# Optimization experiments

Hardware: AMD Instinct MI355X
Metric: run time of the kernel (lower is better)

The kernel has to match this reference:

```python
import jax, jax.numpy as jnp
import numpy as np

B, N, E = 2, 10000, 160000
D, DC, L = 512, 8, 3
EPS = 1e-5


def layer_norm(x, g, b):
    m = jnp.mean(x, axis=-1, keepdims=True)
    v = jnp.mean((x - m) ** 2, axis=-1, keepdims=True)
    return (x - m) * jax.lax.rsqrt(v + EPS) * g + b


def setup_inputs() -> dict:
    key = jax.random.key(0)
    ks = jax.random.split(key, 8)
    node_features = jax.random.normal(ks[0], (B, N, D), dtype=jnp.float32)
    edge_index = jax.random.randint(ks[1], (2, E), 0, N, dtype=jnp.int64)
    edge_attr = jax.random.normal(ks[2], (E, D), dtype=jnp.float32)
    # manifold coordinate projection
    W_coord = jax.random.normal(ks[3], (D, DC), dtype=jnp.float32) / np.sqrt(D)
    # per-layer causal field layers (modeled as linear) and layer norms
    W_field = jax.random.normal(ks[4], (L, D, D), dtype=jnp.float32) / np.sqrt(D)
    b_field = jnp.zeros((L, D), dtype=jnp.float32)
    ln_g = jnp.ones((L, D), dtype=jnp.float32)
    ln_b = jnp.zeros((L, D), dtype=jnp.float32)
    # output projection: LayerNorm + Linear
    out_ln_g = jnp.ones((D,), dtype=jnp.float32)
    out_ln_b = jnp.zeros((D,), dtype=jnp.float32)
    W_out = jax.random.normal(ks[5], (D, D), dtype=jnp.float32) / np.sqrt(D)
    b_out = jnp.zeros((D,), dtype=jnp.float32)
    return dict(node_features=node_features, edge_index=edge_index, edge_attr=edge_attr,
                W_coord=W_coord, W_field=W_field, b_field=b_field, ln_g=ln_g, ln_b=ln_b,
                out_ln_g=out_ln_g, out_ln_b=out_ln_b, W_out=W_out, b_out=b_out)


def reference(node_features, edge_index, edge_attr, W_coord, W_field, b_field,
              ln_g, ln_b, out_ln_g, out_ln_b, W_out, b_out):
    src, dst = edge_index[0], edge_index[1]
    # node coordinates from manifold projection (computed once, from inputs)
    coords = node_features @ W_coord                        # (B, N, DC)
    # transport factor per edge, per batch: exp(-||dst_coord - src_coord||)
    coord_diff = coords[:, dst] - coords[:, src]            # (B, E, DC)
    transport = jnp.exp(-jnp.linalg.norm(coord_diff, axis=-1, keepdims=True))  # (B, E, 1)
    # degree of destination nodes (same for every batch element)
    deg = jnp.zeros((N,), dtype=node_features.dtype).at[dst].add(1.0)
    deg = jnp.clip(deg, 1.0, None)[None, :, None]           # (1, N, 1)

    x = node_features
    edge_msg = None
    for l in range(L):
        x_field = x @ W_field[l] + b_field[l]               # (B, N, D)
        # gather src features, apply transport, add edge attributes
        edge_msg = x_field[:, src] * transport + edge_attr[None]  # (B, E, D)
        # scatter-add into destination nodes, normalize by degree
        upd = jnp.zeros_like(x).at[:, dst].add(edge_msg)    # (B, N, D)
        x = layer_norm(x + upd / deg, ln_g[l], ln_b[l])
    node_output = layer_norm(x, out_ln_g, out_ln_b) @ W_out + b_out
    return node_output, edge_msg
```

## Files before the change

### kernel.cpp

```cpp
#include <hip/hip_runtime.h>
#include <stdint.h>

#define NN 10000
#define EE 160000
#define BB 2
#define DD 512
#define KC 1024
#define MVALID 20000
#define MPAD 20096
#define LEPS 1e-5f

typedef __bf16 bf16_t;
typedef __bf16 bf16x8 __attribute__((ext_vector_type(8)));
typedef __bf16 bf16x4 __attribute__((ext_vector_type(4)));
typedef float f32x4 __attribute__((ext_vector_type(4)));
typedef float f32x2 __attribute__((ext_vector_type(2)));

__device__ inline void gload16(const void* g, void* l) {
  __builtin_amdgcn_global_load_lds((const __attribute__((address_space(1))) uint32_t*)g,
                                   (__attribute__((address_space(3))) uint32_t*)l,
                                   16, 0, 0);
}

__global__ __launch_bounds__(256) void convw_k(const float* __restrict__ Wf,
                                               const float* __restrict__ Wo,
                                               bf16_t* __restrict__ wcat) {
  __shared__ float tile[64][65];
  const int kt = blockIdx.x, nt = blockIdx.y, l = blockIdx.z;
  const float* W = (l < 3) ? (Wf + (size_t)l * 262144) : Wo;
  const int tn = threadIdx.x & 63;
  const int tk = threadIdx.x >> 6;
#pragma unroll
  for (int i = 0; i < 16; i++) {
    const int kl = tk + i * 4;
    tile[kl][tn] = W[(size_t)(kt * 64 + kl) * 512 + nt * 64 + tn];
  }
  __syncthreads();
  const int kl2 = threadIdx.x & 63;
  const int nb = threadIdx.x >> 6;
#pragma unroll
  for (int i = 0; i < 16; i++) {
    const int nl = nb + i * 4;
    bf16_t h = (bf16_t)tile[kl2][nl];
    size_t o = ((size_t)l * 512 + nt * 64 + nl) * 1024 + kt * 64 + kl2;
    wcat[o] = h;
    wcat[o + 512] = h;
  }
}

__global__ __launch_bounds__(256) void coords_k(const float* __restrict__ x,
                                                const float* __restrict__ Wc,
                                                float* __restrict__ out,
                                                bf16_t* __restrict__ xcat) {
  __shared__ float smW[DD * 8];
  for (int i = threadIdx.x; i < DD * 8; i += 256) smW[i] = Wc[i];
  __syncthreads();
  const int wave = threadIdx.x >> 6, lane = threadIdx.x & 63;
  const int n = blockIdx.x * 4 + wave;
  const int b = blockIdx.y;
  const size_t row = (size_t)b * NN + n;
  const float* xr = x + row * DD + lane * 8;
  f32x4 x0 = *(const f32x4*)xr;
  f32x4 x1 = *(const f32x4*)(xr + 4);
  bf16x8 hi, lo;
#pragma unroll
  for (int j = 0; j < 8; j++) {
    float v = (j < 4) ? x0[j] : x1[j - 4];
    bf16_t h = (bf16_t)v;
    hi[j] = h;
    lo[j] = (bf16_t)(v - (float)h);
  }
  bf16_t* xc = xcat + row * KC + lane * 8;
  *(bf16x8*)xc = hi;
  *(bf16x8*)(xc + DD) = lo;
  float a[8];
#pragma unroll
  for (int dc = 0; dc < 8; dc++) a[dc] = 0.f;
#pragma unroll
  for (int j = 0; j < 8; j++) {
    float xv = (j < 4) ? x0[j] : x1[j - 4];
    const float* wrow = smW + (lane * 8 + j) * 8;
#pragma unroll
    for (int dc = 0; dc < 8; dc++) a[dc] += xv * wrow[dc];
  }
#pragma unroll
  for (int dc = 0; dc < 8; dc++)
    for (int o = 32; o >= 1; o >>= 1) a[dc] += __shfl_xor(a[dc], o);
  if (lane == 0) {
#pragma unroll
    for (int dc = 0; dc < 8; dc++) out[row * 8 + dc] = a[dc];
  }
}

__global__ __launch_bounds__(256) void transport_deg_k(const float* __restrict__ coords,
                                                       const int* __restrict__ srcA,
                                                       const int* __restrict__ dstA,
                                                       float* __restrict__ tr,
                                                       int* __restrict__ degc) {
  int e = blockIdx.x * 256 + threadIdx.x;
  int s = srcA[e], d = dstA[e];
#pragma unroll
  for (int b = 0; b < BB; b++) {
    const float* cs = coords + ((size_t)b * NN + s) * 8;
    const float* cd = coords + ((size_t)b * NN + d) * 8;
    float ss = 0.f;
#pragma unroll
    for (int i = 0; i < 8; i++) {
      float df = cd[i] - cs[i];
      ss += df * df;
    }
    tr[(size_t)b * EE + e] = expf(-sqrtf(ss));
  }
  atomicAdd(&degc[d], 1);
}

__global__ __launch_bounds__(1024) void scan_k(const int* __restrict__ cnt, int* __restrict__ rowptr,
                                               float* __restrict__ invdeg) {
  __shared__ int part[1024];
  const int tid = threadIdx.x;
  const int CH = 10;
  int base = tid * CH;
  int local[CH];
  int s = 0;
#pragma unroll
  for (int i = 0; i < CH; i++) {
    int n = base + i;
    int c = (n < NN) ? cnt[n] : 0;
    local[i] = s;
    s += c;
  }
  part[tid] = s;
  __syncthreads();
  for (int off = 1; off < 1024; off <<= 1) {
    int v = (tid >= off) ? part[tid - off] : 0;
    __syncthreads();
    part[tid] += v;
    __syncthreads();
  }
  int excl = (tid > 0) ? part[tid - 1] : 0;
#pragma unroll
  for (int i = 0; i < CH; i++) {
    int n = base + i;
    if (n < NN) {
      rowptr[n] = excl + local[i];
      int c = cnt[n];
      invdeg[n] = 1.0f / (float)(c > 1 ? c : 1);
    }
  }
  if (tid == 0) rowptr[NN] = EE;
}

__global__ __launch_bounds__(256) void fill_k(const int* __restrict__ dstA, const int* __restrict__ rowptr,
                                              int* __restrict__ fill, int* __restrict__ eidA) {
  int e = blockIdx.x * 256 + threadIdx.x;
  int d = dstA[e];
  int pos = rowptr[d] + atomicAdd(&fill[d], 1);
  eidA[pos] = e;
}

__global__ __launch_bounds__(256) void eagg_k(const float* __restrict__ eattr,
                                              const int* __restrict__ rowptr,
                                              const int* __restrict__ eidA,
                                              float* __restrict__ eagg) {
  const int n = blockIdx.x, tid = threadIdx.x;
  const int d0 = tid * 2;
  float a0 = 0.f, a1 = 0.f;
  const int beg = rowptr[n], end = rowptr[n + 1];
  for (int i = beg; i < end; i++) {
    const int e = eidA[i];
    const f32x2 r = __builtin_nontemporal_load((const f32x2*)(eattr + (size_t)e * DD + d0));
    a0 += r[0];
    a1 += r[1];
  }
  f32x2 o;
  o[0] = a0;
  o[1] = a1;
  *(f32x2*)(eagg + (size_t)n * DD + d0) = o;
}

template <bool BF16OUT>
__global__ __launch_bounds__(256) void gemm_bt(const bf16_t* __restrict__ A,
                                               const bf16_t* __restrict__ Bw,
                                               const float* __restrict__ bias,
                                               void* __restrict__ Cv, int mvalid) {
  __shared__ __align__(16) char smem[16384];
  const int tid = threadIdx.x;
  const int lane = tid & 63;
  const int wave = tid >> 6;
  const int mtile = blockIdx.x;
  const int ntile = blockIdx.y;
  const int wr = wave >> 1, wc = wave & 1;

  const int r = tid >> 2;
  const int c = tid & 3;
  const size_t aRow0 = (size_t)(mtile * 128 + r);
  const size_t bRow0 = (size_t)(ntile * 128 + r);
  char* smA = smem;
  char* smB = smem + 8192;
  char* ldsA0 = smA + tid * 16;
  char* ldsA1 = smA + 4096 + tid * 16;
  char* ldsB0 = smB + tid * 16;
  char* ldsB1 = smB + 4096 + tid * 16;

  f32x4 acc[4][4];
#pragma unroll
  for (int m = 0; m < 4; m++)
#pragma unroll
    for (int n = 0; n < 4; n++) acc[m][n] = (f32x4){0.f, 0.f, 0.f, 0.f};

  const int koff = (lane >> 4) * 16;
  const int arow = wr * 64 + (lane & 15);
  const int brow = wc * 64 + (lane & 15);

  for (int kk = 0; kk < KC / 32; ++kk) {
    const int kbase = kk * 32 + c * 8;
    gload16(A + aRow0 * KC + kbase, ldsA0);
    gload16(A + (aRow0 + 64) * KC + kbase, ldsA1);
    gload16(Bw + bRow0 * KC + kbase, ldsB0);
    gload16(Bw + (bRow0 + 64) * KC + kbase, ldsB1);
    __syncthreads();
    bf16x8 af[4], bfr[4];
#pragma unroll
    for (int m = 0; m < 4; m++) af[m] = *(const bf16x8*)(smA + (arow + m * 16) * 64 + koff);
#pragma unroll
    for (int n = 0; n < 4; n++) bfr[n] = *(const bf16x8*)(smB + (brow + n * 16) * 64 + koff);
#pragma unroll
    for (int m = 0; m < 4; m++)
#pragma unroll
      for (int n = 0; n < 4; n++)
        acc[m][n] = __builtin_amdgcn_mfma_f32_16x16x32_bf16(af[m], bfr[n], acc[m][n], 0, 0, 0);
    __syncthreads();
  }

  const int crow0 = mtile * 128 + wr * 64 + (lane >> 4) * 4;
  const int ccol0 = ntile * 128 + wc * 64 + (lane & 15);
#pragma unroll
  for (int n = 0; n < 4; n++) {
    const int col = ccol0 + n * 16;
    const float bv = bias[col];
#pragma unroll
    for (int m = 0; m < 4; m++) {
      const int rw = crow0 + m * 16;
#pragma unroll
      for (int j = 0; j < 4; j++) {
        int rowi = rw + j;
        if (rowi < mvalid) {
          const float v = acc[m][n][j] + bv;
          if constexpr (BF16OUT)
            ((bf16_t*)Cv)[(size_t)rowi * DD + col] = (bf16_t)v;
          else
            ((float*)Cv)[(size_t)rowi * DD + col] = v;
        }
      }
    }
  }
}

__global__ __launch_bounds__(64) void layer_k(const bf16_t* __restrict__ xfield,
                                              const float* __restrict__ xprev0, int is_l0,
                                              bf16_t* __restrict__ xcat,
                                              const float* __restrict__ transport,
                                              const int* __restrict__ srcA,
                                              const int* __restrict__ rowptr,
                                              const int* __restrict__ eidA,
                                              const float* __restrict__ eagg,
                                              const float* __restrict__ invdeg,
                                              const float* __restrict__ g,
                                              const float* __restrict__ bbias) {
  const int n = blockIdx.x, b = blockIdx.y, lane = threadIdx.x;
  const size_t row = (size_t)b * NN + n;
  const int d0 = lane * 8;
  float acc[8];
#pragma unroll
  for (int j = 0; j < 8; j++) acc[j] = 0.f;
  const int beg = rowptr[n], end = rowptr[n + 1];
  const float* trb = transport + (size_t)b * EE;
  const bf16_t* xfb = xfield + (size_t)b * NN * DD;
  for (int i = beg; i < end; i++) {
    const int e = eidA[i];
    const int s = srcA[e];
    const float tr = trb[e];
    const bf16x8 xv = *(const bf16x8*)(xfb + (size_t)s * DD + d0);
#pragma unroll
    for (int j = 0; j < 8; j++) acc[j] += (float)xv[j] * tr;
  }
  bf16_t* xc = xcat + row * KC + d0;
  float xp[8];
  if (is_l0) {
    const f32x4 p0 = *(const f32x4*)(xprev0 + row * DD + d0);
    const f32x4 p1 = *(const f32x4*)(xprev0 + row * DD + d0 + 4);
#pragma unroll
    for (int j = 0; j < 8; j++) xp[j] = (j < 4) ? p0[j] : p1[j - 4];
  } else {
    const bf16x8 hi = *(const bf16x8*)(xc);
    const bf16x8 lo = *(const bf16x8*)(xc + DD);
#pragma unroll
    for (int j = 0; j < 8; j++) xp[j] = (float)hi[j] + (float)lo[j];
  }
  const f32x4 e0 = *(const f32x4*)(eagg + (size_t)n * DD + d0);
  const f32x4 e1 = *(const f32x4*)(eagg + (size_t)n * DD + d0 + 4);
  const float idg = invdeg[n];
  float v[8];
  float s1 = 0.f, s2 = 0.f;
#pragma unroll
  for (int j = 0; j < 8; j++) {
    const float ea = (j < 4) ? e0[j] : e1[j - 4];
    v[j] = xp[j] + (acc[j] + ea) * idg;
    s1 += v[j];
    s2 += v[j] * v[j];
  }
#pragma unroll
  for (int o = 32; o >= 1; o >>= 1) {
    s1 += __shfl_xor(s1, o);
    s2 += __shfl_xor(s2, o);
  }
  const float mean = s1 * (1.f / 512.f);
  const float var = s2 * (1.f / 512.f) - mean * mean;
  const float rs = rsqrtf(var + LEPS);
  const f32x4 g0 = *(const f32x4*)(g + d0);
  const f32x4 g1 = *(const f32x4*)(g + d0 + 4);
  const f32x4 b0 = *(const f32x4*)(bbias + d0);
  const f32x4 b1 = *(const f32x4*)(bbias + d0 + 4);
  bf16x8 ho, lo2;
#pragma unroll
  for (int j = 0; j < 8; j++) {
    const float gg = (j < 4) ? g0[j] : g1[j - 4];
    const float bb = (j < 4) ? b0[j] : b1[j - 4];
    const float y = (v[j] - mean) * rs * gg + bb;
    bf16_t h = (bf16_t)y;
    ho[j] = h;
    lo2[j] = (bf16_t)(y - (float)h);
  }
  *(bf16x8*)xc = ho;
  *(bf16x8*)(xc + DD) = lo2;
}

__global__ __launch_bounds__(256) void edgemsg_k(const bf16_t* __restrict__ xfield,
                                                 const float* __restrict__ transport,
                                                 const int* __restrict__ srcA,
                                                 const float* __restrict__ eattr,
                                                 float* __restrict__ out) {
  const int wv = threadIdx.x >> 6, lane = threadIdx.x & 63;
  const int e = blockIdx.x * 4 + wv;
  const int d0 = lane * 8;
  const int s = srcA[e];
  const f32x4 a0 = __builtin_nontemporal_load((const f32x4*)(eattr + (size_t)e * DD + d0));
  const f32x4 a1 = __builtin_nontemporal_load((const f32x4*)(eattr + (size_t)e * DD + d0 + 4));
  const float t0 = transport[e];
  const float t1 = transport[(size_t)EE + e];
  const bf16x8 x0 = *(const bf16x8*)(xfield + (size_t)s * DD + d0);
  const bf16x8 x1 = *(const bf16x8*)(xfield + ((size_t)NN + s) * DD + d0);
  f32x4 o00, o01, o10, o11;
#pragma unroll
  for (int j = 0; j < 4; j++) {
    o00[j] = (float)x0[j] * t0 + a0[j];
    o01[j] = (float)x0[j + 4] * t0 + a1[j];
    o10[j] = (float)x1[j] * t1 + a0[j];
    o11[j] = (float)x1[j + 4] * t1 + a1[j];
  }
  float* ob0 = out + (size_t)e * DD + d0;
  float* ob1 = out + ((size_t)EE + e) * DD + d0;
  __builtin_nontemporal_store(o00, (f32x4*)ob0);
  __builtin_nontemporal_store(o01, (f32x4*)(ob0 + 4));
  __builtin_nontemporal_store(o10, (f32x4*)ob1);
  __builtin_nontemporal_store(o11, (f32x4*)(ob1 + 4));
}

__global__ __launch_bounds__(64) void outln_k(bf16_t* __restrict__ xcat,
                                              const float* __restrict__ g,
                                              const float* __restrict__ bbias) {
  const int n = blockIdx.x, b = blockIdx.y, lane = threadIdx.x;
  const size_t row = (size_t)b * NN + n;
  const int d0 = lane * 8;
  bf16_t* xc = xcat + row * KC + d0;
  const bf16x8 hi = *(const bf16x8*)(xc);
  const bf16x8 lo = *(const bf16x8*)(xc + DD);
  float v[8];
  float s1 = 0.f, s2 = 0.f;
#pragma unroll
  for (int j = 0; j < 8; j++) {
    v[j] = (float)hi[j] + (float)lo[j];
    s1 += v[j];
    s2 += v[j] * v[j];
  }
#pragma unroll
  for (int o = 32; o >= 1; o >>= 1) {
    s1 += __shfl_xor(s1, o);
    s2 += __shfl_xor(s2, o);
  }
  const float mean = s1 * (1.f / 512.f);
  const float var = s2 * (1.f / 512.f) - mean * mean;
  const float rs = rsqrtf(var + LEPS);
  const f32x4 g0 = *(const f32x4*)(g + d0);
  const f32x4 g1 = *(const f32x4*)(g + d0 + 4);
  const f32x4 b0 = *(const f32x4*)(bbias + d0);
  const f32x4 b1 = *(const f32x4*)(bbias + d0 + 4);
  bf16x8 ho, lo2;
#pragma unroll
  for (int j = 0; j < 8; j++) {
    const float gg = (j < 4) ? g0[j] : g1[j - 4];
    const float bb = (j < 4) ? b0[j] : b1[j - 4];
    const float y = (v[j] - mean) * rs * gg + bb;
    bf16_t h = (bf16_t)y;
    ho[j] = h;
    lo2[j] = (bf16_t)(y - (float)h);
  }
  *(bf16x8*)xc = ho;
  *(bf16x8*)(xc + DD) = lo2;
}

extern "C" void kernel_launch(void* const* d_in, const int* in_sizes, int n_in,
                              void* d_out, int out_size, void* d_ws, size_t ws_size,
                              hipStream_t stream) {
  const float* nf = (const float*)d_in[0];
  const int* eidx = (const int*)d_in[1];
  const float* eattr = (const float*)d_in[2];
  const float* Wc = (const float*)d_in[3];
  const float* Wf = (const float*)d_in[4];
  const float* bfield = (const float*)d_in[5];
  const float* lng = (const float*)d_in[6];
  const float* lnb = (const float*)d_in[7];
  const float* olng = (const float*)d_in[8];
  const float* olnb = (const float*)d_in[9];
  const float* Wo = (const float*)d_in[10];
  const float* bo = (const float*)d_in[11];
  const int* srcA = eidx;
  const int* dstA = eidx + EE;
  float* outp = (float*)d_out;

  char* ws = (char*)d_ws;
  size_t off = 0;
  auto alloc = [&](size_t bytes) {
    void* p = ws + off;
    off += (bytes + 255) & ~(size_t)255;
    return p;
  };
  bf16_t* xcat = (bf16_t*)alloc((size_t)MPAD * KC * 2);
  bf16_t* xfield = (bf16_t*)alloc((size_t)MPAD * DD * 2);
  bf16_t* wcat = (bf16_t*)alloc((size_t)4 * DD * KC * 2);
  float* eagg = (float*)alloc((size_t)NN * DD * 4);
  float* coords = (float*)alloc((size_t)BB * NN * 8 * 4);
  float* transport = (float*)alloc((size_t)BB * EE * 4);
  int* degc = (int*)alloc(NN * 4);
  int* rowptr = (int*)alloc((NN + 1) * 4);
  int* fillb = (int*)alloc(NN * 4);
  int* eidl = (int*)alloc(EE * 4);
  float* invdeg = (float*)alloc(NN * 4);

  hipMemsetAsync(degc, 0, NN * 4, stream);
  hipMemsetAsync(fillb, 0, NN * 4, stream);
  hipMemsetAsync(xcat + (size_t)MVALID * KC, 0, (size_t)(MPAD - MVALID) * KC * 2, stream);

  convw_k<<<dim3(8, 8, 4), 256, 0, stream>>>(Wf, Wo, wcat);
  coords_k<<<dim3(2500, 2), 256, 0, stream>>>(nf, Wc, coords, xcat);
  transport_deg_k<<<625, 256, 0, stream>>>(coords, srcA, dstA, transport, degc);
  scan_k<<<1, 1024, 0, stream>>>(degc, rowptr, invdeg);
  fill_k<<<625, 256, 0, stream>>>(dstA, rowptr, fillb, eidl);
  eagg_k<<<10000, 256, 0, stream>>>(eattr, rowptr, eidl, eagg);

  for (int l = 0; l < 3; l++) {
    gemm_bt<true><<<dim3(157, 4), 256, 0, stream>>>(xcat, wcat + (size_t)l * DD * KC,
                                                    bfield + l * DD, xfield, MPAD);
    if (l == 2)
      edgemsg_k<<<40000, 256, 0, stream>>>(xfield, transport, srcA, eattr,
                                           outp + (size_t)BB * NN * DD);
    layer_k<<<dim3(NN, 2), 64, 0, stream>>>(xfield, nf, (l == 0) ? 1 : 0, xcat, transport, srcA,
                                            rowptr, eidl, eagg, invdeg, lng + l * DD,
                                            lnb + l * DD);
  }
  outln_k<<<dim3(NN, 2), 64, 0, stream>>>(xcat, olng, olnb);
  gemm_bt<false><<<dim3(157, 4), 256, 0, stream>>>(xcat, wcat + (size_t)3 * DD * KC, bo, outp,
                                                   MVALID);
}
```

Before: 751.6 us.

## Fold output LayerNorm into final GEMM and restructure layer aggregation

Folds the output LayerNorm gamma into the converted output weight and its beta into a precomputed bias (beta·W_out + b_out). The last layer kernel then writes mean-subtracted activations plus a per-row rstd that the final GEMM applies in its epilogue, which removes the separate outln pass. Edge source ids and transport factors pre-scaled by inverse degree are permuted into CSR order, so the gather no longer goes through two indirections. Each wave now processes both batch elements for one node, loading indices cooperatively and broadcasting them by shuffle. The cost is extra preprocessing kernels and a float atomic accumulation for the folded bias, whose summation order is not fixed.

Result: faster. 736.9 us (-2.0%).

```diff
diff --git a/kernel.cpp b/kernel.cpp
--- a/kernel.cpp
+++ b/kernel.cpp
@@ -12,7 +12,6 @@
 
 typedef __bf16 bf16_t;
 typedef __bf16 bf16x8 __attribute__((ext_vector_type(8)));
-typedef __bf16 bf16x4 __attribute__((ext_vector_type(4)));
 typedef float f32x4 __attribute__((ext_vector_type(4)));
 typedef float f32x2 __attribute__((ext_vector_type(2)));
 
@@ -24,6 +23,7 @@
 
 __global__ __launch_bounds__(256) void convw_k(const float* __restrict__ Wf,
                                                const float* __restrict__ Wo,
+                                               const float* __restrict__ olng,
                                                bf16_t* __restrict__ wcat) {
   __shared__ float tile[64][65];
   const int kt = blockIdx.x, nt = blockIdx.y, l = blockIdx.z;
@@ -38,13 +38,32 @@
   __syncthreads();
   const int kl2 = threadIdx.x & 63;
   const int nb = threadIdx.x >> 6;
+  const float gk = (l == 3) ? olng[kt * 64 + kl2] : 1.0f;
 #pragma unroll
   for (int i = 0; i < 16; i++) {
     const int nl = nb + i * 4;
-    bf16_t h = (bf16_t)tile[kl2][nl];
+    bf16_t h = (bf16_t)(tile[kl2][nl] * gk);
     size_t o = ((size_t)l * 512 + nt * 64 + nl) * 1024 + kt * 64 + kl2;
     wcat[o] = h;
     wcat[o + 512] = h;
+  }
+}
+
+__global__ __launch_bounds__(512) void ubinit_k(const float* __restrict__ bo, float* __restrict__ ub) {
+  ub[threadIdx.x] = bo[threadIdx.x];
+}
+__global__ __launch_bounds__(256) void ubacc_k(const float* __restrict__ olnb,
+                                               const float* __restrict__ Wo,
+                                               float* __restrict__ ub) {
+  const int k0 = blockIdx.x * 16;
+  const int tid = threadIdx.x;
+#pragma unroll
+  for (int h = 0; h < 2; h++) {
+    const int n = tid + h * 256;
+    float s = 0.f;
+#pragma unroll
+    for (int kk = 0; kk < 16; kk++) s += olnb[k0 + kk] * Wo[(size_t)(k0 + kk) * 512 + n];
+    atomicAdd(&ub[n], s);
   }
 }
 
@@ -158,9 +177,26 @@
   eidA[pos] = e;
 }
 
+__global__ __launch_bounds__(256) void remap_k(const int* __restrict__ eidA,
+                                               const int* __restrict__ srcA,
+                                               const int* __restrict__ dstA,
+                                               const float* __restrict__ tr,
+                                               const float* __restrict__ invdeg,
+                                               int* __restrict__ srcs,
+                                               float* __restrict__ trs) {
+  int i = blockIdx.x * 256 + threadIdx.x;
+  const int e = eidA[i];
+  const int s = srcA[e];
+  const float idg = invdeg[dstA[e]];
+  srcs[i] = s;
+  trs[i] = tr[e] * idg;
+  trs[(size_t)EE + i] = tr[(size_t)EE + e] * idg;
+}
+
 __global__ __launch_bounds__(256) void eagg_k(const float* __restrict__ eattr,
                                               const int* __restrict__ rowptr,
                                               const int* __restrict__ eidA,
+                                              const float* __restrict__ invdeg,
                                               float* __restrict__ eagg) {
   const int n = blockIdx.x, tid = threadIdx.x;
   const int d0 = tid * 2;
@@ -172,17 +208,19 @@
     a0 += r[0];
     a1 += r[1];
   }
+  const float idg = invdeg[n];
   f32x2 o;
-  o[0] = a0;
-  o[1] = a1;
+  o[0] = a0 * idg;
+  o[1] = a1 * idg;
   *(f32x2*)(eagg + (size_t)n * DD + d0) = o;
 }
 
-template <bool BF16OUT>
+template <int MODE>
 __global__ __launch_bounds__(256) void gemm_bt(const bf16_t* __restrict__ A,
                                                const bf16_t* __restrict__ Bw,
                                                const float* __restrict__ bias,
-                                               void* __restrict__ Cv, int mvalid) {
+                                               void* __restrict__ Cv, int mvalid,
+                                               const float* __restrict__ rs) {
   __shared__ __align__(16) char smem[16384];
   const int tid = threadIdx.x;
   const int lane = tid & 63;
@@ -245,94 +283,162 @@
       for (int j = 0; j < 4; j++) {
         int rowi = rw + j;
         if (rowi < mvalid) {
-          const float v = acc[m][n][j] + bv;
-          if constexpr (BF16OUT)
-            ((bf16_t*)Cv)[(size_t)rowi * DD + col] = (bf16_t)v;
+          if constexpr (MODE == 0)
+            ((bf16_t*)Cv)[(size_t)rowi * DD + col] = (bf16_t)(acc[m][n][j] + bv);
           else
-            ((float*)Cv)[(size_t)rowi * DD + col] = v;
+            ((float*)Cv)[(size_t)rowi * DD + col] = acc[m][n][j] * rs[rowi] + bv;
         }
       }
     }
   }
 }
 
-__global__ __launch_bounds__(64) void layer_k(const bf16_t* __restrict__ xfield,
-                                              const float* __restrict__ xprev0, int is_l0,
-                                              bf16_t* __restrict__ xcat,
-                                              const float* __restrict__ transport,
-                                              const int* __restrict__ srcA,
-                                              const int* __restrict__ rowptr,
-                                              const int* __restrict__ eidA,
-                                              const float* __restrict__ eagg,
-                                              const float* __restrict__ invdeg,
-                                              const float* __restrict__ g,
-                                              const float* __restrict__ bbias) {
-  const int n = blockIdx.x, b = blockIdx.y, lane = threadIdx.x;
-  const size_t row = (size_t)b * NN + n;
+__global__ __launch_bounds__(256) void layer_k(const bf16_t* __restrict__ xfield,
+                                               const float* __restrict__ nf, int is_l0, int outstat,
+                                               bf16_t* __restrict__ xcat,
+                                               const int* __restrict__ srcs,
+                                               const float* __restrict__ trs,
+                                               const int* __restrict__ rowptr,
+                                               const float* __restrict__ eagg,
+                                               const float* __restrict__ g,
+                                               const float* __restrict__ bbias,
+                                               float* __restrict__ rs_out) {
+  const int wave = threadIdx.x >> 6, lane = threadIdx.x & 63;
+  const int n = blockIdx.x * 4 + wave;
   const int d0 = lane * 8;
-  float acc[8];
-#pragma unroll
-  for (int j = 0; j < 8; j++) acc[j] = 0.f;
   const int beg = rowptr[n], end = rowptr[n + 1];
-  const float* trb = transport + (size_t)b * EE;
-  const bf16_t* xfb = xfield + (size_t)b * NN * DD;
-  for (int i = beg; i < end; i++) {
-    const int e = eidA[i];
-    const int s = srcA[e];
-    const float tr = trb[e];
-    const bf16x8 xv = *(const bf16x8*)(xfb + (size_t)s * DD + d0);
-#pragma unroll
-    for (int j = 0; j < 8; j++) acc[j] += (float)xv[j] * tr;
-  }
-  bf16_t* xc = xcat + row * KC + d0;
-  float xp[8];
+  const bf16_t* xf0 = xfield + (size_t)0 * NN * DD + d0;
+  const bf16_t* xf1 = xfield + (size_t)1 * NN * DD + d0;
+  const float* trs1p = trs + EE;
+  float acc0[8], acc1[8];
+#pragma unroll
+  for (int j = 0; j < 8; j++) acc0[j] = acc1[j] = 0.f;
+
+  for (int c0 = beg; c0 < end; c0 += 64) {
+    const int cnt = min(64, end - c0);
+    int s_r = 0;
+    float t0_r = 0.f, t1_r = 0.f;
+    if (lane < cnt) {
+      s_r = srcs[c0 + lane];
+      t0_r = trs[c0 + lane];
+      t1_r = trs1p[c0 + lane];
+    }
+    for (int j = 0; j < cnt; j++) {
+      const int s = __shfl(s_r, j);
+      const float t0 = __shfl(t0_r, j);
+      const float t1 = __shfl(t1_r, j);
+      const bf16x8 xv0 = *(const bf16x8*)(xf0 + (size_t)s * DD);
+      const bf16x8 xv1 = *(const bf16x8*)(xf1 + (size_t)s * DD);
+#pragma unroll
+      for (int q = 0; q < 8; q++) {
+        acc0[q] += t0 * (float)xv0[q];
+        acc1[q] += t1 * (float)xv1[q];
+      }
+    }
+  }
+
+  bf16_t* xc0 = xcat + (size_t)n * KC + d0;
+  bf16_t* xc1 = xcat + (size_t)(NN + n) * KC + d0;
+  float xp0[8], xp1[8];
   if (is_l0) {
-    const f32x4 p0 = *(const f32x4*)(xprev0 + row * DD + d0);
-    const f32x4 p1 = *(const f32x4*)(xprev0 + row * DD + d0 + 4);
-#pragma unroll
-    for (int j = 0; j < 8; j++) xp[j] = (j < 4) ? p0[j] : p1[j - 4];
+    const f32x4 p00 = *(const f32x4*)(nf + (size_t)n * DD + d0);
+    const f32x4 p01 = *(const f32x4*)(nf + (size_t)n * DD + d0 + 4);
+    const f32x4 p10 = *(const f32x4*)(nf + (size_t)(NN + n) * DD + d0);
+    const f32x4 p11 = *(const f32x4*)(nf + (size_t)(NN + n) * DD + d0 + 4);
+#pragma unroll
+    for (int j = 0; j < 8; j++) {
+      xp0[j] = (j < 4) ? p00[j] : p01[j - 4];
+      xp1[j] = (j < 4) ? p10[j] : p11[j - 4];
+    }
   } else {
-    const bf16x8 hi = *(const bf16x8*)(xc);
-    const bf16x8 lo = *(const bf16x8*)(xc + DD);
-#pragma unroll
-    for (int j = 0; j < 8; j++) xp[j] = (float)hi[j] + (float)lo[j];
+    const bf16x8 h0 = *(const bf16x8*)(xc0);
+    const bf16x8 l0v = *(const bf16x8*)(xc0 + DD);
+    const bf16x8 h1 = *(const bf16x8*)(xc1);
+    const bf16x8 l1v = *(const bf16x8*)(xc1 + DD);
+#pragma unroll
+    for (int j = 0; j < 8; j++) {
+      xp0[j] = (float)h0[j] + (float)l0v[j];
+      xp1[j] = (float)h1[j] + (float)l1v[j];
+    }
   }
   const f32x4 e0 = *(const f32x4*)(eagg + (size_t)n * DD + d0);
   const f32x4 e1 = *(const f32x4*)(eagg + (size_t)n * DD + d0 + 4);
-  const float idg = invdeg[n];
-  float v[8];
-  float s1 = 0.f, s2 = 0.f;
+  float v0[8], v1[8];
+  float s10 = 0.f, s20 = 0.f, s11 = 0.f, s21 = 0.f;
 #pragma unroll
   for (int j = 0; j < 8; j++) {
     const float ea = (j < 4) ? e0[j] : e1[j - 4];
-    v[j] = xp[j] + (acc[j] + ea) * idg;
-    s1 += v[j];
-    s2 += v[j] * v[j];
+    v0[j] = xp0[j] + acc0[j] + ea;
+    v1[j] = xp1[j] + acc1[j] + ea;
+    s10 += v0[j];
+    s20 += v0[j] * v0[j];
+    s11 += v1[j];
+    s21 += v1[j] * v1[j];
   }
 #pragma unroll
   for (int o = 32; o >= 1; o >>= 1) {
-    s1 += __shfl_xor(s1, o);
-    s2 += __shfl_xor(s2, o);
-  }
-  const float mean = s1 * (1.f / 512.f);
-  const float var = s2 * (1.f / 512.f) - mean * mean;
-  const float rs = rsqrtf(var + LEPS);
+    s10 += __shfl_xor(s10, o);
+    s20 += __shfl_xor(s20, o);
+    s11 += __shfl_xor(s11, o);
+    s21 += __shfl_xor(s21, o);
+  }
+  const float mean0 = s10 * (1.f / 512.f);
+  const float rs0 = rsqrtf(s20 * (1.f / 512.f) - mean0 * mean0 + LEPS);
+  const float mean1 = s11 * (1.f / 512.f);
+  const float rs1 = rsqrtf(s21 * (1.f / 512.f) - mean1 * mean1 + LEPS);
   const f32x4 g0 = *(const f32x4*)(g + d0);
   const f32x4 g1 = *(const f32x4*)(g + d0 + 4);
   const f32x4 b0 = *(const f32x4*)(bbias + d0);
   const f32x4 b1 = *(const f32x4*)(bbias + d0 + 4);
-  bf16x8 ho, lo2;
+  float y0[8], y1[8];
+  float sy10 = 0.f, sy20 = 0.f, sy11 = 0.f, sy21 = 0.f;
 #pragma unroll
   for (int j = 0; j < 8; j++) {
     const float gg = (j < 4) ? g0[j] : g1[j - 4];
     const float bb = (j < 4) ? b0[j] : b1[j - 4];
-    const float y = (v[j] - mean) * rs * gg + bb;
-    bf16_t h = (bf16_t)y;
-    ho[j] = h;
-    lo2[j] = (bf16_t)(y - (float)h);
-  }
-  *(bf16x8*)xc = ho;
-  *(bf16x8*)(xc + DD) = lo2;
+    y0[j] = (v0[j] - mean0) * rs0 * gg + bb;
+    y1[j] = (v1[j] - mean1) * rs1 * gg + bb;
+    sy10 += y0[j];
+    sy20 += y0[j] * y0[j];
+    sy11 += y1[j];
+    sy21 += y1[j] * y1[j];
+  }
+  float sub0 = 0.f, sub1 = 0.f;
+  if (outstat) {
+#pragma unroll
+    for (int o = 32; o >= 1; o >>= 1) {
+      sy10 += __shfl_xor(sy10, o);
+      sy20 += __shfl_xor(sy20, o);
+      sy11 += __shfl_xor(sy11, o);
+      sy21 += __shfl_xor(sy21, o);
+    }
+    const float my0 = sy10 * (1.f / 512.f);
+    const float rsy0 = rsqrtf(sy20 * (1.f / 512.f) - my0 * my0 + LEPS);
+    const float my1 = sy11 * (1.f / 512.f);
+    const float rsy1 = rsqrtf(sy21 * (1.f / 512.f) - my1 * my1 + LEPS);
+    if (lane == 0) {
+      rs_out[n] = rsy0;
+      rs_out[NN + n] = rsy1;
+    }
+    sub0 = my0;
+    sub1 = my1;
+  }
+  bf16x8 ho0, lo0, ho1, lo1;
+#pragma unroll
+  for (int j = 0; j < 8; j++) {
+    const float ya = y0[j] - sub0;
+    const float yb = y1[j] - sub1;
+    bf16_t ha = (bf16_t)ya;
+    bf16_t hb = (bf16_t)yb;
+    ho0[j] = ha;
+    lo0[j] = (bf16_t)(ya - (float)ha);
+    ho1[j] = hb;
+    lo1[j] = (bf16_t)(yb - (float)hb);
+  }
+  *(bf16x8*)xc0 = ho0;
+  *(bf16x8*)(xc0 + DD) = lo0;
+  *(bf16x8*)xc1 = ho1;
+  *(bf16x8*)(xc1 + DD) = lo1;
 }
 
 __global__ __launch_bounds__(256) void edgemsg_k(const bf16_t* __restrict__ xfield,
@@ -364,49 +470,6 @@
   __builtin_nontemporal_store(o01, (f32x4*)(ob0 + 4));
   __builtin_nontemporal_store(o10, (f32x4*)ob1);
   __builtin_nontemporal_store(o11, (f32x4*)(ob1 + 4));
-}
-
-__global__ __launch_bounds__(64) void outln_k(bf16_t* __restrict__ xcat,
-                                              const float* __restrict__ g,
-                                              const float* __restrict__ bbias) {
-  const int n = blockIdx.x, b = blockIdx.y, lane = threadIdx.x;
-  const size_t row = (size_t)b * NN + n;
-  const int d0 = lane * 8;
-  bf16_t* xc = xcat + row * KC + d0;
-  const bf16x8 hi = *(const bf16x8*)(xc);
-  const bf16x8 lo = *(const bf16x8*)(xc + DD);
-  float v[8];
-  float s1 = 0.f, s2 = 0.f;
-#pragma unroll
-  for (int j = 0; j < 8; j++) {
-    v[j] = (float)hi[j] + (float)lo[j];
-    s1 += v[j];
-    s2 += v[j] * v[j];
-  }
-#pragma unroll
-  for (int o = 32; o >= 1; o >>= 1) {
-    s1 += __shfl_xor(s1, o);
-    s2 += __shfl_xor(s2, o);
-  }
-  const float mean = s1 * (1.f / 512.f);
-  const float var = s2 * (1.f / 512.f) - mean * mean;
-  const float rs = rsqrtf(var + LEPS);
-  const f32x4 g0 = *(const f32x4*)(g + d0);
-  const f32x4 g1 = *(const f32x4*)(g + d0 + 4);
-  const f32x4 b0 = *(const f32x4*)(bbias + d0);
-  const f32x4 b1 = *(const f32x4*)(bbias + d0 + 4);
-  bf16x8 ho, lo2;
-#pragma unroll
-  for (int j = 0; j < 8; j++) {
-    const float gg = (j < 4) ? g0[j] : g1[j - 4];
-    const float bb = (j < 4) ? b0[j] : b1[j - 4];
-    const float y = (v[j] - mean) * rs * gg + bb;
-    bf16_t h = (bf16_t)y;
-    ho[j] = h;
-    lo2[j] = (bf16_t)(y - (float)h);
-  }
-  *(bf16x8*)xc = ho;
-  *(bf16x8*)(xc + DD) = lo2;
 }
 
 extern "C" void kernel_launch(void* const* d_in, const int* in_sizes, int n_in,
@@ -441,34 +504,39 @@
   float* eagg = (float*)alloc((size_t)NN * DD * 4);
   float* coords = (float*)alloc((size_t)BB * NN * 8 * 4);
   float* transport = (float*)alloc((size_t)BB * EE * 4);
+  float* trs = (float*)alloc((size_t)BB * EE * 4);
+  int* srcs = (int*)alloc(EE * 4);
   int* degc = (int*)alloc(NN * 4);
   int* rowptr = (int*)alloc((NN + 1) * 4);
   int* fillb = (int*)alloc(NN * 4);
   int* eidl = (int*)alloc(EE * 4);
   float* invdeg = (float*)alloc(NN * 4);
+  float* rs_out = (float*)alloc((size_t)BB * NN * 4);
+  float* ub = (float*)alloc(DD * 4);
 
   hipMemsetAsync(degc, 0, NN * 4, stream);
   hipMemsetAsync(fillb, 0, NN * 4, stream);
   hipMemsetAsync(xcat + (size_t)MVALID * KC, 0, (size_t)(MPAD - MVALID) * KC * 2, stream);
 
-  convw_k<<<dim3(8, 8, 4), 256, 0, stream>>>(Wf, Wo, wcat);
+  convw_k<<<dim3(8, 8, 4), 256, 0, stream>>>(Wf, Wo, olng, wcat);
+  ubinit_k<<<1, 512, 0, stream>>>(bo, ub);
+  ubacc_k<<<32, 256, 0, stream>>>(olnb, Wo, ub);
   coords_k<<<dim3(2500, 2), 256, 0, stream>>>(nf, Wc, coords, xcat);
   transport_deg_k<<<625, 256, 0, stream>>>(coords, srcA, dstA, transport, degc);
   scan_k<<<1, 1024, 0, stream>>>(degc, rowptr, invdeg);
   fill_k<<<625, 256, 0, stream>>>(dstA, rowptr, fillb, eidl);
-  eagg_k<<<10000, 256, 0, stream>>>(eattr, rowptr, eidl, eagg);
+  remap_k<<<625, 256, 0, stream>>>(eidl, srcA, dstA, transport, invdeg, srcs, trs);
+  eagg_k<<<10000, 256, 0, stream>>>(eattr, rowptr, eidl, invdeg, eagg);
 
   for (int l = 0; l < 3; l++) {
-    gemm_bt<true><<<dim3(157, 4), 256, 0, stream>>>(xcat, wcat + (size_t)l * DD * KC,
-                                                    bfield + l * DD, xfield, MPAD);
+    gemm_bt<0><<<dim3(157, 4), 256, 0, stream>>>(xcat, wcat + (size_t)l * DD * KC,
+                                                 bfield + l * DD, xfield, MVALID, nullptr);
     if (l == 2)
       edgemsg_k<<<40000, 256, 0, stream>>>(xfield, transport, srcA, eattr,
                                            outp + (size_t)BB * NN * DD);
-    layer_k<<<dim3(NN, 2), 64, 0, stream>>>(xfield, nf, (l == 0) ? 1 : 0, xcat, transport, srcA,
-                                            rowptr, eidl, eagg, invdeg, lng + l * DD,
-                                            lnb + l * DD);
-  }
-  outln_k<<<dim3(NN, 2), 64, 0, stream>>>(xcat, olng, olnb);
-  gemm_bt<false><<<dim3(157, 4), 256, 0, stream>>>(xcat, wcat + (size_t)3 * DD * KC, bo, outp,
-                                                   MVALID);
-}
+    layer_k<<<2500, 256, 0, stream>>>(xfield, nf, (l == 0) ? 1 : 0, (l == 2) ? 1 : 0, xcat, srcs,
+                                      trs, rowptr, eagg, lng + l * DD, lnb + l * DD, rs_out);
+  }
+  gemm_bt<1><<<dim3(157, 4), 256, 0, stream>>>(xcat, wcat + (size_t)3 * DD * KC, ub, outp, MVALID,
+                                               rs_out);
+}
```
